# Kernel optimization log

Hardware: AMD Instinct MI355X
Metric: run time of the kernel (lower is better)

## Reference

```python
import jax, jax.numpy as jnp
import numpy as np

B, N, D, E, FF, K = 2, 1024, 768, 8, 4, 2
H = D * FF  # 3072


def _xavier_uniform(key, shape, gain=1.0):
    # shape is (..., out, in) like torch Linear weight; fan_in/out from last two dims
    fan_out, fan_in = shape[-2], shape[-1]
    limit = gain * np.sqrt(6.0 / (fan_in + fan_out))
    return jax.random.uniform(key, shape, jnp.float32, -limit, limit)


def setup_inputs() -> dict:
    key = jax.random.key(0)
    ks = jax.random.split(key, 5)
    tokens = jax.random.normal(ks[0], (B, N, D), jnp.float32)
    # Token-choice top-K routing: softmax over experts, keep top-K weights
    logits = jax.random.normal(ks[1], (B, N, E), jnp.float32)
    probs = jax.nn.softmax(logits, axis=-1)
    topv, topi = jax.lax.top_k(probs, K)              # (B,N,K)
    onehot = jax.nn.one_hot(topi, E, dtype=jnp.float32)  # (B,N,K,E)
    combine_weights = jnp.einsum('bnk,bnke->bne', topv, onehot)  # (B,N,E)
    dispatch_weights = (combine_weights > 0).astype(jnp.float32)
    # Stacked expert weights (torch Linear convention: W is (out, in), y = x @ W.T)
    Wg = _xavier_uniform(ks[2], (E, H, D))
    Wv = _xavier_uniform(ks[3], (E, H, D))
    Wo = _xavier_uniform(ks[4], (E, D, H), gain=0.02)
    scale = jnp.full((E,), 1.0 / E, jnp.float32)  # output_scale init = 1/E
    return dict(tokens=tokens, dispatch_weights=dispatch_weights,
                combine_weights=combine_weights, Wg=Wg, Wv=Wv, Wo=Wo, scale=scale)


def reference(tokens, dispatch_weights, combine_weights, Wg, Wv, Wo, scale):
    Bb, Nn, Dd = tokens.shape
    Ee = Wg.shape[0]
    x = tokens.reshape(Bb * Nn, Dd)                    # (T, D)
    mask = (dispatch_weights.reshape(-1, Ee) > 0).astype(x.dtype)  # (T, E)
    comb = combine_weights.reshape(-1, Ee) * mask      # zero where not dispatched
    # SwiGLU-style expert FFN, all experts in one grouped contraction
    gate = jax.nn.gelu(jnp.einsum('td,ehd->teh', x, Wg), approximate=False)  # (T,E,H)
    value = jnp.einsum('td,ehd->teh', x, Wv)           # (T,E,H)
    expert_out = jnp.einsum('teh,edh->ted', gate * value, Wo) * scale[None, :, None]  # (T,E,D)
    # Weighted combine: sum_e comb[t,e] * expert_out[t,e,:]
    y = jnp.einsum('ted,te->td', expert_out, comb)     # (T, D)
    return y.reshape(Bb, Nn, Dd)
```

## Files before the change

### kernel.cpp

```cpp
#include <hip/hip_runtime.h>
#include <hip/hip_bf16.h>
#include <math.h>

#define T_TOK 2048
#define DIM   768
#define NEXP  8
#define HDIM  3072
#define MAXP  (T_TOK * 2)
#define LDST  40
#define NTILE_MAX 40

typedef __attribute__((ext_vector_type(8))) short bfrag;
typedef __attribute__((ext_vector_type(4))) float f32x4;

__device__ __forceinline__ unsigned short f2bf(float f) {
  union { float f; unsigned int u; } x; x.f = f;
  unsigned int r = x.u + 0x7fffu + ((x.u >> 16) & 1u);
  return (unsigned short)(r >> 16);
}

__global__ void k_prep(const float* __restrict__ disp,
                       const float* __restrict__ comb,
                       int* __restrict__ meta,
                       float* __restrict__ row_comb,
                       int* __restrict__ row_token,
                       int* __restrict__ tok2pair,
                       const float* __restrict__ X, unsigned short* __restrict__ Xb,
                       const float* __restrict__ Wg, const float* __restrict__ Wv,
                       const float* __restrict__ Wo,
                       unsigned short* __restrict__ Wgh, unsigned short* __restrict__ Wvh,
                       unsigned short* __restrict__ Woh) {
  __shared__ int s_wsum[4];
  int b = blockIdx.x;
  int tid = threadIdx.x;
  if (b == 0) {
    int lane = tid & 63, wid = tid >> 6;
    unsigned long long lmask = (1ull << lane) - 1ull;
    int tn0 = 0, tn1 = 0, tn2 = 0, tn3 = 0, tn4 = 0, tn5 = 0, tn6 = 0, tn7 = 0;
    int run = 0;
#pragma unroll
    for (int e = 0; e < NEXP; ++e) {
      int off_e = run;
#pragma unroll
      for (int it = 0; it < 8; ++it) {
        int t = it * 256 + tid;
        bool pos = disp[t * NEXP + e] > 0.f;
        unsigned long long m = __ballot(pos);
        int lpfx = (int)__popcll(m & lmask);
        int wcnt = (int)__popcll(m);
        if (lane == 0) s_wsum[wid] = wcnt;
        __syncthreads();
        int w0 = s_wsum[0], w1 = s_wsum[1], w2 = s_wsum[2], w3 = s_wsum[3];
        int wbase = run + (wid > 0 ? w0 : 0) + (wid > 1 ? w1 : 0) + (wid > 2 ? w2 : 0);
        if (pos) {
          int p = wbase + lpfx;
          row_token[p] = t;
          row_comb[p] = comb[t * NEXP + e];
          int sl;
          if      (it == 0) { sl = tn0++; }
          else if (it == 1) { sl = tn1++; }
          else if (it == 2) { sl = tn2++; }
          else if (it == 3) { sl = tn3++; }
          else if (it == 4) { sl = tn4++; }
          else if (it == 5) { sl = tn5++; }
          else if (it == 6) { sl = tn6++; }
          else              { sl = tn7++; }
          tok2pair[t * 2 + sl] = p;
        }
        run += w0 + w1 + w2 + w3;
        __syncthreads();
      }
      if (tid == 0) { meta[e] = run - off_e; meta[NEXP + e] = off_e; }
    }
    if (tid == 0) {
      int nt = 0;
      for (int e = 0; e < NEXP; ++e) {
        int cnt = meta[e];
        for (int m0 = 0; m0 < cnt; m0 += 128)
          meta[17 + nt++] = (e << 16) | (m0 >> 7);
      }
      meta[16] = nt;
    }
    return;
  }
  int idx = b - 1;
  const float* src;
  unsigned short* dst;
  if (idx < 48)        { src = X;  dst = Xb;  }
  else if (idx < 624)  { src = Wg; dst = Wgh; idx -= 48;   }
  else if (idx < 1200) { src = Wv; dst = Wvh; idx -= 624;  }
  else                 { src = Wo; dst = Woh; idx -= 1200; }
  size_t base = (size_t)idx * 32768 + (size_t)tid * 8;
#pragma unroll
  for (int g = 0; g < 4; ++g) {
    float4 va[4], vb[4];
#pragma unroll
    for (int u = 0; u < 4; ++u) {
      size_t i = base + (size_t)(g * 4 + u) * 2048;
      va[u] = *(const float4*)(src + i);
      vb[u] = *(const float4*)(src + i + 4);
    }
#pragma unroll
    for (int u = 0; u < 4; ++u) {
      size_t i = base + (size_t)(g * 4 + u) * 2048;
      unsigned short r[8];
      r[0]=f2bf(va[u].x); r[1]=f2bf(va[u].y); r[2]=f2bf(va[u].z); r[3]=f2bf(va[u].w);
      r[4]=f2bf(vb[u].x); r[5]=f2bf(vb[u].y); r[6]=f2bf(vb[u].z); r[7]=f2bf(vb[u].w);
      *(uint4*)(dst + i) = *(uint4*)r;
    }
  }
}

template<int WBF>
__global__ __launch_bounds__(256, 2) void k_gemm_gv_t(
    const unsigned short* __restrict__ Xb,
    const float* __restrict__ Wg,
    const float* __restrict__ Wv,
    const unsigned short* __restrict__ Wgh,
    const unsigned short* __restrict__ Wvh,
    const int* __restrict__ meta,
    const int* __restrict__ row_token,
    unsigned short* __restrict__ ubuf)
{
  int blk = blockIdx.x;
  int xc = blk & 7, slot = blk >> 3;
  int nt = xc + 8 * (slot / NTILE_MAX);
  int t  = slot % NTILE_MAX;
  if (t >= meta[16]) return;
  int tv = meta[17 + t];
  int e = tv >> 16, m0 = (tv & 0xffff) << 7;
  int cnt = meta[e], off = meta[NEXP + e];
  int n0 = nt * 128;

  __shared__ unsigned short As[128 * LDST];
  __shared__ unsigned short Bgs[128 * LDST];
  __shared__ unsigned short Bvs[128 * LDST];

  int tid = threadIdx.x;
  int wid = tid >> 6, lane = tid & 63;
  int wm = (wid >> 1) * 64, wn = (wid & 1) * 64;
  int lr = lane & 15, quad = lane >> 4;

  int a_tok[2];
#pragma unroll
  for (int r = 0; r < 2; ++r) {
    int row = (tid + 256 * r) >> 2;
    int gr = m0 + row; if (gr >= cnt) gr = cnt - 1;
    a_tok[r] = row_token[off + gr];
  }

  const float* Wgb = Wg + (size_t)e * ((size_t)HDIM * DIM);
  const float* Wvb = Wv + (size_t)e * ((size_t)HDIM * DIM);
  const unsigned short* Wghb = Wgh + (size_t)e * ((size_t)HDIM * DIM);
  const unsigned short* Wvhb = Wvh + (size_t)e * ((size_t)HDIM * DIM);

  f32x4 zero4 = {0.f, 0.f, 0.f, 0.f};
  f32x4 accg[4][4], accv[4][4];
#pragma unroll
  for (int i = 0; i < 4; ++i)
#pragma unroll
    for (int j = 0; j < 4; ++j) { accg[i][j] = zero4; accv[i][j] = zero4; }

  for (int k0 = 0; k0 < DIM; k0 += 32) {
    __syncthreads();
#pragma unroll
    for (int r = 0; r < 2; ++r) {
      int c2 = tid + 256 * r;
      int row = c2 >> 2, sub = c2 & 3;
      uint4 av = *(const uint4*)(Xb + (size_t)a_tok[r] * DIM + k0 + sub * 8);
      *(uint4*)(&As[row * LDST + sub * 8]) = av;
    }
    if constexpr (WBF) {
#pragma unroll
      for (int r = 0; r < 2; ++r) {
        int c2 = tid + 256 * r;
        int row = c2 >> 2, sub = c2 & 3;
        uint4 gv = *(const uint4*)(Wghb + (size_t)(n0 + row) * DIM + k0 + sub * 8);
        *(uint4*)(&Bgs[row * LDST + sub * 8]) = gv;
        uint4 vv = *(const uint4*)(Wvhb + (size_t)(n0 + row) * DIM + k0 + sub * 8);
        *(uint4*)(&Bvs[row * LDST + sub * 8]) = vv;
      }
    } else {
#pragma unroll
      for (int r = 0; r < 4; ++r) {
        int c2 = tid + 256 * r;
        int row = c2 >> 3, c4 = c2 & 7;
        float4 gv = *(const float4*)(Wgb + (size_t)(n0 + row) * DIM + k0 + c4 * 4);
        ushort4 gp;
        gp.x = f2bf(gv.x); gp.y = f2bf(gv.y); gp.z = f2bf(gv.z); gp.w = f2bf(gv.w);
        *(ushort4*)(&Bgs[row * LDST + c4 * 4]) = gp;
        float4 vv = *(const float4*)(Wvb + (size_t)(n0 + row) * DIM + k0 + c4 * 4);
        ushort4 vp;
        vp.x = f2bf(vv.x); vp.y = f2bf(vv.y); vp.z = f2bf(vv.z); vp.w = f2bf(vv.w);
        *(ushort4*)(&Bvs[row * LDST + c4 * 4]) = vp;
      }
    }
    __syncthreads();
    bfrag a[4], bg[4], bv[4];
#pragma unroll
    for (int i = 0; i < 4; ++i)
      a[i] = *(const bfrag*)(&As[(wm + i * 16 + lr) * LDST + quad * 8]);
#pragma unroll
    for (int j = 0; j < 4; ++j) {
      bg[j] = *(const bfrag*)(&Bgs[(wn + j * 16 + lr) * LDST + quad * 8]);
      bv[j] = *(const bfrag*)(&Bvs[(wn + j * 16 + lr) * LDST + quad * 8]);
    }
#pragma unroll
    for (int i = 0; i < 4; ++i)
#pragma unroll
      for (int j = 0; j < 4; ++j) {
        accg[i][j] = __builtin_amdgcn_mfma_f32_16x16x32_bf16(a[i], bg[j], accg[i][j], 0, 0, 0);
        accv[i][j] = __builtin_amdgcn_mfma_f32_16x16x32_bf16(a[i], bv[j], accv[i][j], 0, 0, 0);
      }
  }

#pragma unroll
  for (int i = 0; i < 4; ++i)
#pragma unroll
    for (int rg = 0; rg < 4; ++rg) {
      int gr = m0 + wm + i * 16 + quad * 4 + rg;
      if (gr < cnt) {
        size_t base = (size_t)(off + gr) * HDIM + n0 + wn;
#pragma unroll
        for (int j = 0; j < 4; ++j) {
          float g = accg[i][j][rg];
          float v = accv[i][j][rg];
          float u = 0.5f * g * (1.0f + erff(g * 0.70710678118654752f)) * v;
          ubuf[base + j * 16 + lr] = f2bf(u);
        }
      }
    }
}

template<int WBF>
__global__ __launch_bounds__(256, 2) void k_gemm_out_t(
    const unsigned short* __restrict__ U,
    const float* __restrict__ Wo,
    const unsigned short* __restrict__ Woh,
    const float* __restrict__ scale,
    const int* __restrict__ meta,
    const int* __restrict__ row_token,
    const float* __restrict__ row_comb,
    float* __restrict__ partial,
    float* __restrict__ out,
    int mode)
{
  int blk = blockIdx.x;
  int xc = blk & 7, slot = blk >> 3;
  int sidx = xc + 8 * (slot / NTILE_MAX);
  int nt = sidx % 6, ks = sidx / 6;
  int t = slot % NTILE_MAX;
  if (t >= meta[16]) return;
  int tv = meta[17 + t];
  int e = tv >> 16, m0 = (tv & 0xffff) << 7;
  int cnt = meta[e], off = meta[NEXP + e];
  int n0 = nt * 128;
  int kbase = ks * (HDIM / 4);

  __shared__ unsigned short As[128 * LDST];
  __shared__ unsigned short Bs[128 * LDST];

  int tid = threadIdx.x;
  int wid = tid >> 6, lane = tid & 63;
  int wm = (wid >> 1) * 64, wn = (wid & 1) * 64;
  int lr = lane & 15, quad = lane >> 4;

  int a_grow[2];
#pragma unroll
  for (int r = 0; r < 2; ++r) {
    int row = (tid + 256 * r) >> 2;
    int gr = m0 + row; if (gr >= cnt) gr = cnt - 1;
    a_grow[r] = off + gr;
  }

  const float* Wb = Wo + (size_t)e * ((size_t)DIM * HDIM);
  const unsigned short* Wbh = Woh + (size_t)e * ((size_t)DIM * HDIM);

  f32x4 zero4 = {0.f, 0.f, 0.f, 0.f};
  f32x4 acc[4][4];
#pragma unroll
  for (int i = 0; i < 4; ++i)
#pragma unroll
    for (int j = 0; j < 4; ++j) acc[i][j] = zero4;

  for (int kk = 0; kk < HDIM / 4; kk += 32) {
    int k0 = kbase + kk;
    __syncthreads();
#pragma unroll
    for (int r = 0; r < 2; ++r) {
      int c2 = tid + 256 * r;
      int row = c2 >> 2, sub = c2 & 3;
      uint4 av = *(const uint4*)(U + (size_t)a_grow[r] * HDIM + k0 + sub * 8);
      *(uint4*)(&As[row * LDST + sub * 8]) = av;
    }
    if constexpr (WBF) {
#pragma unroll
      for (int r = 0; r < 2; ++r) {
        int c2 = tid + 256 * r;
        int row = c2 >> 2, sub = c2 & 3;
        uint4 bv = *(const uint4*)(Wbh + (size_t)(n0 + row) * HDIM + k0 + sub * 8);
        *(uint4*)(&Bs[row * LDST + sub * 8]) = bv;
      }
    } else {
#pragma unroll
      for (int r = 0; r < 4; ++r) {
        int c2 = tid + 256 * r;
        int row = c2 >> 3, c4 = c2 & 7;
        float4 bvv = *(const float4*)(Wb + (size_t)(n0 + row) * HDIM + k0 + c4 * 4);
        ushort4 bp;
        bp.x = f2bf(bvv.x); bp.y = f2bf(bvv.y); bp.z = f2bf(bvv.z); bp.w = f2bf(bvv.w);
        *(ushort4*)(&Bs[row * LDST + c4 * 4]) = bp;
      }
    }
    __syncthreads();
    bfrag a[4], b[4];
#pragma unroll
    for (int i = 0; i < 4; ++i)
      a[i] = *(const bfrag*)(&As[(wm + i * 16 + lr) * LDST + quad * 8]);
#pragma unroll
    for (int j = 0; j < 4; ++j)
      b[j] = *(const bfrag*)(&Bs[(wn + j * 16 + lr) * LDST + quad * 8]);
#pragma unroll
    for (int i = 0; i < 4; ++i)
#pragma unroll
      for (int j = 0; j < 4; ++j)
        acc[i][j] = __builtin_amdgcn_mfma_f32_16x16x32_bf16(a[i], b[j], acc[i][j], 0, 0, 0);
  }

  float sc = scale[e];
#pragma unroll
  for (int i = 0; i < 4; ++i)
#pragma unroll
    for (int rg = 0; rg < 4; ++rg) {
      int gr = m0 + wm + i * 16 + quad * 4 + rg;
      if (gr < cnt) {
        int grow = off + gr;
        float w = row_comb[grow] * sc;
        if (mode == 0) {
          float* pb = partial + ((size_t)ks * MAXP + grow) * DIM + n0 + wn;
#pragma unroll
          for (int j = 0; j < 4; ++j)
            pb[j * 16 + lr] = acc[i][j][rg] * w;
        } else {
          int tok = row_token[grow];
          float* ob = out + (size_t)tok * DIM + n0 + wn;
#pragma unroll
          for (int j = 0; j < 4; ++j)
            atomicAdd(ob + j * 16 + lr, acc[i][j][rg] * w);
        }
      }
    }
}

__global__ void k_combine(const float* __restrict__ partial,
                          const int* __restrict__ tok2pair,
                          float* __restrict__ out) {
  int idx = blockIdx.x * 256 + threadIdx.x;
  int t = idx / 192, d4 = idx % 192;
  int p0 = tok2pair[t * 2], p1 = tok2pair[t * 2 + 1];
  float sx = 0.f, sy = 0.f, sz = 0.f, sw = 0.f;
#pragma unroll
  for (int ks = 0; ks < 4; ++ks) {
    float4 a = *(const float4*)(partial + ((size_t)ks * MAXP + p0) * DIM + d4 * 4);
    float4 b = *(const float4*)(partial + ((size_t)ks * MAXP + p1) * DIM + d4 * 4);
    sx += a.x + b.x; sy += a.y + b.y; sz += a.z + b.z; sw += a.w + b.w;
  }
  float4 r; r.x = sx; r.y = sy; r.z = sz; r.w = sw;
  *(float4*)(out + (size_t)t * DIM + d4 * 4) = r;
}

extern "C" void kernel_launch(void* const* d_in, const int* in_sizes, int n_in,
                              void* d_out, int out_size, void* d_ws, size_t ws_size,
                              hipStream_t stream) {
  const float* tokens = (const float*)d_in[0];
  const float* disp   = (const float*)d_in[1];
  const float* comb   = (const float*)d_in[2];
  const float* Wg     = (const float*)d_in[3];
  const float* Wv     = (const float*)d_in[4];
  const float* Wo     = (const float*)d_in[5];
  const float* scale  = (const float*)d_in[6];
  float* out = (float*)d_out;

  char* ws = (char*)d_ws;
  int*   meta      = (int*)ws;
  int*   row_token = (int*)(ws + 16384);
  float* row_comb  = (float*)(ws + 32768);
  int*   tok2pair  = (int*)(ws + 49152);
  unsigned short* Xb   = (unsigned short*)(ws + (1ull << 20));
  unsigned short* ubuf = (unsigned short*)(ws + (5ull << 20));
  float* partial = (float*)(ws + (32ull << 20));

  const size_t need_partial = (32ull << 20) + (size_t)4 * MAXP * DIM * sizeof(float);
  const size_t need_full = 188ull << 20;
  const size_t need_mid  = 140ull << 20;

  int wbf, mode;
  unsigned short *Wgh = nullptr, *Wvh = nullptr, *Woh = nullptr;
  if (ws_size >= need_full) {
    wbf = 1; mode = 0;
    Wgh = (unsigned short*)(ws + (80ull  << 20));
    Wvh = (unsigned short*)(ws + (116ull << 20));
    Woh = (unsigned short*)(ws + (152ull << 20));
  } else if (ws_size >= need_mid) {
    wbf = 1; mode = 1;
    Wgh = (unsigned short*)(ws + (32ull  << 20));
    Wvh = (unsigned short*)(ws + (68ull  << 20));
    Woh = (unsigned short*)(ws + (104ull << 20));
  } else {
    wbf = 0;
    mode = (ws_size >= need_partial) ? 0 : 1;
    Wgh = Wvh = Woh = (unsigned short*)Xb;
  }

  int prep_grid = wbf ? (1 + 48 + 3 * 576) : (1 + 48);
  hipLaunchKernelGGL(k_prep, dim3(prep_grid), dim3(256), 0, stream,
                     disp, comb, meta, row_comb, row_token, tok2pair,
                     tokens, Xb, Wg, Wv, Wo, Wgh, Wvh, Woh);

  if (wbf)
    hipLaunchKernelGGL(HIP_KERNEL_NAME(k_gemm_gv_t<1>), dim3(NTILE_MAX * 24), dim3(256), 0, stream,
                       Xb, Wg, Wv, Wgh, Wvh, meta, row_token, ubuf);
  else
    hipLaunchKernelGGL(HIP_KERNEL_NAME(k_gemm_gv_t<0>), dim3(NTILE_MAX * 24), dim3(256), 0, stream,
                       Xb, Wg, Wv, Wgh, Wvh, meta, row_token, ubuf);

  if (mode == 1)
    hipMemsetAsync(d_out, 0, (size_t)out_size * sizeof(float), stream);

  if (wbf)
    hipLaunchKernelGGL(HIP_KERNEL_NAME(k_gemm_out_t<1>), dim3(NTILE_MAX * 6 * 4), dim3(256), 0, stream,
                       ubuf, Wo, Woh, scale, meta, row_token, row_comb, partial, out, mode);
  else
    hipLaunchKernelGGL(HIP_KERNEL_NAME(k_gemm_out_t<0>), dim3(NTILE_MAX * 6 * 4), dim3(256), 0, stream,
                       ubuf, Wo, Woh, scale, meta, row_token, row_comb, partial, out, mode);

  if (mode == 0)
    hipLaunchKernelGGL(k_combine, dim3((T_TOK * DIM / 4) / 256), dim3(256), 0, stream,
                       partial, tok2pair, out);
}
```

Measured before the change: 401.1 us.

## Stage GEMM tiles via direct global-to-LDS loads with XOR-swizzled unpadded layout

Replaces the register round-trip for loading A and B tiles into shared memory with global_load_lds direct-to-LDS transfers in both expert GEMM kernels. The padded LDS row stride is replaced by an unpadded 32-element stride with an XOR swizzle on 16-byte chunks, so the writes stay contiguous per wave while fragment reads avoid bank conflicts. The output GEMM's launch bound is raised to three blocks per SM. This aims to cut VGPR pressure and instruction overhead on loads and to reduce LDS use, at the cost of relying on exact swizzle and lane-ordering correctness for the direct LDS writes.

Result: no change. 401.3 us (+0.1%).

```diff
diff --git a/kernel.cpp b/kernel.cpp
--- a/kernel.cpp
+++ b/kernel.cpp
@@ -7,7 +7,6 @@
 #define NEXP  8
 #define HDIM  3072
 #define MAXP  (T_TOK * 2)
-#define LDST  40
 #define NTILE_MAX 40
 
 typedef __attribute__((ext_vector_type(8))) short bfrag;
@@ -17,6 +16,12 @@
   union { float f; unsigned int u; } x; x.f = f;
   unsigned int r = x.u + 0x7fffu + ((x.u >> 16) & 1u);
   return (unsigned short)(r >> 16);
+}
+
+__device__ __forceinline__ void gload16(const void* g, void* lds_uniform) {
+  __builtin_amdgcn_global_load_lds(
+      (const __attribute__((address_space(1))) void*)g,
+      (__attribute__((address_space(3))) void*)lds_uniform, 16, 0, 0);
 }
 
 __global__ void k_prep(const float* __restrict__ disp,
@@ -111,6 +116,7 @@
   }
 }
 
+
 template<int WBF>
 __global__ __launch_bounds__(256, 2) void k_gemm_gv_t(
     const unsigned short* __restrict__ Xb,
@@ -123,28 +129,32 @@
     unsigned short* __restrict__ ubuf)
 {
   int blk = blockIdx.x;
-  int xc = blk & 7, slot = blk >> 3;
-  int nt = xc + 8 * (slot / NTILE_MAX);
-  int t  = slot % NTILE_MAX;
+  int xc = blk & 7, slot0 = blk >> 3;
+  int nt = xc + 8 * (slot0 / NTILE_MAX);
+  int t  = slot0 % NTILE_MAX;
   if (t >= meta[16]) return;
   int tv = meta[17 + t];
   int e = tv >> 16, m0 = (tv & 0xffff) << 7;
   int cnt = meta[e], off = meta[NEXP + e];
   int n0 = nt * 128;
 
-  __shared__ unsigned short As[128 * LDST];
-  __shared__ unsigned short Bgs[128 * LDST];
-  __shared__ unsigned short Bvs[128 * LDST];
+  __shared__ unsigned short As[128 * 32];
+  __shared__ unsigned short Bgs[128 * 32];
+  __shared__ unsigned short Bvs[128 * 32];
 
   int tid = threadIdx.x;
   int wid = tid >> 6, lane = tid & 63;
   int wm = (wid >> 1) * 64, wn = (wid & 1) * 64;
   int lr = lane & 15, quad = lane >> 4;
-
-  int a_tok[2];
+  int qx = ((quad ^ (lr ^ (lr >> 2))) & 3) * 8;
+
+  int srow[2], ssub[2], a_tok[2];
 #pragma unroll
   for (int r = 0; r < 2; ++r) {
-    int row = (tid + 256 * r) >> 2;
+    int s = tid + 256 * r;
+    int row = s >> 2, sub = s & 3;
+    srow[r] = row;
+    ssub[r] = sub ^ ((row ^ (row >> 2)) & 3);
     int gr = m0 + row; if (gr >= cnt) gr = cnt - 1;
     a_tok[r] = row_token[off + gr];
   }
@@ -163,47 +173,46 @@
 
   for (int k0 = 0; k0 < DIM; k0 += 32) {
     __syncthreads();
-#pragma unroll
-    for (int r = 0; r < 2; ++r) {
-      int c2 = tid + 256 * r;
-      int row = c2 >> 2, sub = c2 & 3;
-      uint4 av = *(const uint4*)(Xb + (size_t)a_tok[r] * DIM + k0 + sub * 8);
-      *(uint4*)(&As[row * LDST + sub * 8]) = av;
-    }
     if constexpr (WBF) {
 #pragma unroll
       for (int r = 0; r < 2; ++r) {
-        int c2 = tid + 256 * r;
-        int row = c2 >> 2, sub = c2 & 3;
-        uint4 gv = *(const uint4*)(Wghb + (size_t)(n0 + row) * DIM + k0 + sub * 8);
-        *(uint4*)(&Bgs[row * LDST + sub * 8]) = gv;
-        uint4 vv = *(const uint4*)(Wvhb + (size_t)(n0 + row) * DIM + k0 + sub * 8);
-        *(uint4*)(&Bvs[row * LDST + sub * 8]) = vv;
+        int lb = (r * 256 + wid * 64) * 8;
+        gload16(Xb  + (size_t)a_tok[r] * DIM        + k0 + ssub[r] * 8, &As[lb]);
+        gload16(Wghb + (size_t)(n0 + srow[r]) * DIM + k0 + ssub[r] * 8, &Bgs[lb]);
+        gload16(Wvhb + (size_t)(n0 + srow[r]) * DIM + k0 + ssub[r] * 8, &Bvs[lb]);
       }
     } else {
+#pragma unroll
+      for (int r = 0; r < 2; ++r) {
+        int sub = (tid + 256 * r) & 3;
+        uint4 av = *(const uint4*)(Xb + (size_t)a_tok[r] * DIM + k0 + sub * 8);
+        *(uint4*)(&As[srow[r] * 32 + ssub[r] * 8]) = av;
+      }
 #pragma unroll
       for (int r = 0; r < 4; ++r) {
         int c2 = tid + 256 * r;
         int row = c2 >> 3, c4 = c2 & 7;
-        float4 gv = *(const float4*)(Wgb + (size_t)(n0 + row) * DIM + k0 + c4 * 4);
+        int sz2 = (row ^ (row >> 2)) & 3;
+        int c4s = (((c4 >> 1) ^ sz2) << 1) | (c4 & 1);
+        float4 gvv = *(const float4*)(Wgb + (size_t)(n0 + row) * DIM + k0 + c4 * 4);
         ushort4 gp;
-        gp.x = f2bf(gv.x); gp.y = f2bf(gv.y); gp.z = f2bf(gv.z); gp.w = f2bf(gv.w);
-        *(ushort4*)(&Bgs[row * LDST + c4 * 4]) = gp;
-        float4 vv = *(const float4*)(Wvb + (size_t)(n0 + row) * DIM + k0 + c4 * 4);
+        gp.x = f2bf(gvv.x); gp.y = f2bf(gvv.y); gp.z = f2bf(gvv.z); gp.w = f2bf(gvv.w);
+        *(ushort4*)(&Bgs[row * 32 + c4s * 4]) = gp;
+        float4 vvv = *(const float4*)(Wvb + (size_t)(n0 + row) * DIM + k0 + c4 * 4);
         ushort4 vp;
-        vp.x = f2bf(vv.x); vp.y = f2bf(vv.y); vp.z = f2bf(vv.z); vp.w = f2bf(vv.w);
-        *(ushort4*)(&Bvs[row * LDST + c4 * 4]) = vp;
+        vp.x = f2bf(vvv.x); vp.y = f2bf(vvv.y); vp.z = f2bf(vvv.z); vp.w = f2bf(vvv.w);
+        *(ushort4*)(&Bvs[row * 32 + c4s * 4]) = vp;
       }
     }
     __syncthreads();
     bfrag a[4], bg[4], bv[4];
 #pragma unroll
     for (int i = 0; i < 4; ++i)
-      a[i] = *(const bfrag*)(&As[(wm + i * 16 + lr) * LDST + quad * 8]);
+      a[i] = *(const bfrag*)(&As[(wm + i * 16 + lr) * 32 + qx]);
 #pragma unroll
     for (int j = 0; j < 4; ++j) {
-      bg[j] = *(const bfrag*)(&Bgs[(wn + j * 16 + lr) * LDST + quad * 8]);
-      bv[j] = *(const bfrag*)(&Bvs[(wn + j * 16 + lr) * LDST + quad * 8]);
+      bg[j] = *(const bfrag*)(&Bgs[(wn + j * 16 + lr) * 32 + qx]);
+      bv[j] = *(const bfrag*)(&Bvs[(wn + j * 16 + lr) * 32 + qx]);
     }
 #pragma unroll
     for (int i = 0; i < 4; ++i)
@@ -233,7 +242,7 @@
 }
 
 template<int WBF>
-__global__ __launch_bounds__(256, 2) void k_gemm_out_t(
+__global__ __launch_bounds__(256, 3) void k_gemm_out_t(
     const unsigned short* __restrict__ U,
     const float* __restrict__ Wo,
     const unsigned short* __restrict__ Woh,
@@ -246,10 +255,10 @@
     int mode)
 {
   int blk = blockIdx.x;
-  int xc = blk & 7, slot = blk >> 3;
-  int sidx = xc + 8 * (slot / NTILE_MAX);
+  int xc = blk & 7, slot0 = blk >> 3;
+  int sidx = xc + 8 * (slot0 / NTILE_MAX);
   int nt = sidx % 6, ks = sidx / 6;
-  int t = slot % NTILE_MAX;
+  int t = slot0 % NTILE_MAX;
   if (t >= meta[16]) return;
   int tv = meta[17 + t];
   int e = tv >> 16, m0 = (tv & 0xffff) << 7;
@@ -257,18 +266,22 @@
   int n0 = nt * 128;
   int kbase = ks * (HDIM / 4);
 
-  __shared__ unsigned short As[128 * LDST];
-  __shared__ unsigned short Bs[128 * LDST];
+  __shared__ unsigned short As[128 * 32];
+  __shared__ unsigned short Bs[128 * 32];
 
   int tid = threadIdx.x;
   int wid = tid >> 6, lane = tid & 63;
   int wm = (wid >> 1) * 64, wn = (wid & 1) * 64;
   int lr = lane & 15, quad = lane >> 4;
-
-  int a_grow[2];
+  int qx = ((quad ^ (lr ^ (lr >> 2))) & 3) * 8;
+
+  int srow[2], ssub[2], a_grow[2];
 #pragma unroll
   for (int r = 0; r < 2; ++r) {
-    int row = (tid + 256 * r) >> 2;
+    int s = tid + 256 * r;
+    int row = s >> 2, sub = s & 3;
+    srow[r] = row;
+    ssub[r] = sub ^ ((row ^ (row >> 2)) & 3);
     int gr = m0 + row; if (gr >= cnt) gr = cnt - 1;
     a_grow[r] = off + gr;
   }
@@ -286,40 +299,40 @@
   for (int kk = 0; kk < HDIM / 4; kk += 32) {
     int k0 = kbase + kk;
     __syncthreads();
-#pragma unroll
-    for (int r = 0; r < 2; ++r) {
-      int c2 = tid + 256 * r;
-      int row = c2 >> 2, sub = c2 & 3;
-      uint4 av = *(const uint4*)(U + (size_t)a_grow[r] * HDIM + k0 + sub * 8);
-      *(uint4*)(&As[row * LDST + sub * 8]) = av;
-    }
     if constexpr (WBF) {
 #pragma unroll
       for (int r = 0; r < 2; ++r) {
-        int c2 = tid + 256 * r;
-        int row = c2 >> 2, sub = c2 & 3;
-        uint4 bv = *(const uint4*)(Wbh + (size_t)(n0 + row) * HDIM + k0 + sub * 8);
-        *(uint4*)(&Bs[row * LDST + sub * 8]) = bv;
+        int lb = (r * 256 + wid * 64) * 8;
+        gload16(U   + (size_t)a_grow[r] * HDIM      + k0 + ssub[r] * 8, &As[lb]);
+        gload16(Wbh + (size_t)(n0 + srow[r]) * HDIM + k0 + ssub[r] * 8, &Bs[lb]);
       }
     } else {
+#pragma unroll
+      for (int r = 0; r < 2; ++r) {
+        int sub = (tid + 256 * r) & 3;
+        uint4 av = *(const uint4*)(U + (size_t)a_grow[r] * HDIM + k0 + sub * 8);
+        *(uint4*)(&As[srow[r] * 32 + ssub[r] * 8]) = av;
+      }
 #pragma unroll
       for (int r = 0; r < 4; ++r) {
         int c2 = tid + 256 * r;
         int row = c2 >> 3, c4 = c2 & 7;
+        int sz2 = (row ^ (row >> 2)) & 3;
+        int c4s = (((c4 >> 1) ^ sz2) << 1) | (c4 & 1);
         float4 bvv = *(const float4*)(Wb + (size_t)(n0 + row) * HDIM + k0 + c4 * 4);
         ushort4 bp;
         bp.x = f2bf(bvv.x); bp.y = f2bf(bvv.y); bp.z = f2bf(bvv.z); bp.w = f2bf(bvv.w);
-        *(ushort4*)(&Bs[row * LDST + c4 * 4]) = bp;
+        *(ushort4*)(&Bs[row * 32 + c4s * 4]) = bp;
       }
     }
     __syncthreads();
     bfrag a[4], b[4];
 #pragma unroll
     for (int i = 0; i < 4; ++i)
-      a[i] = *(const bfrag*)(&As[(wm + i * 16 + lr) * LDST + quad * 8]);
+      a[i] = *(const bfrag*)(&As[(wm + i * 16 + lr) * 32 + qx]);
 #pragma unroll
     for (int j = 0; j < 4; ++j)
-      b[j] = *(const bfrag*)(&Bs[(wn + j * 16 + lr) * LDST + quad * 8]);
+      b[j] = *(const bfrag*)(&Bs[(wn + j * 16 + lr) * 32 + qx]);
 #pragma unroll
     for (int i = 0; i < 4; ++i)
 #pragma unroll
```
